# Performance work log

Hardware: AMD Instinct MI355X
Metric: run time of the kernel (lower is better)

The kernel has to match this reference:

```python
import jax, jax.numpy as jnp
import numpy as np

D_MODEL = 1024
N_HEADS = 16
D_K = D_MODEL // N_HEADS
D_FF = 4096
B, S = 4, 2048


def setup_inputs() -> dict:
    key = jax.random.key(0)
    ks = jax.random.split(key, 16)
    s = 0.02
    inp = {
        "x": jax.random.normal(ks[0], (B, S, D_MODEL), dtype=jnp.float32),
        "wq": jax.random.normal(ks[1], (D_MODEL, D_MODEL), dtype=jnp.float32) * s,
        "bq": jnp.zeros((D_MODEL,), jnp.float32),
        "wk": jax.random.normal(ks[2], (D_MODEL, D_MODEL), dtype=jnp.float32) * s,
        "bk": jnp.zeros((D_MODEL,), jnp.float32),
        "wv": jax.random.normal(ks[3], (D_MODEL, D_MODEL), dtype=jnp.float32) * s,
        "bv": jnp.zeros((D_MODEL,), jnp.float32),
        "wo": jax.random.normal(ks[4], (D_MODEL, D_MODEL), dtype=jnp.float32) * s,
        "bo": jnp.zeros((D_MODEL,), jnp.float32),
        "w1": jax.random.normal(ks[5], (D_MODEL, D_FF), dtype=jnp.float32) * s,
        "b1": jnp.zeros((D_FF,), jnp.float32),
        "w2": jax.random.normal(ks[6], (D_FF, D_MODEL), dtype=jnp.float32) * s,
        "b2": jnp.zeros((D_MODEL,), jnp.float32),
        "ln1_g": jnp.ones((D_MODEL,), jnp.float32),
        "ln1_b": jnp.zeros((D_MODEL,), jnp.float32),
        "ln2_g": jnp.ones((D_MODEL,), jnp.float32),
        "ln2_b": jnp.zeros((D_MODEL,), jnp.float32),
    }
    return inp


def _layernorm(x, g, b, eps=1e-5):
    mu = jnp.mean(x, axis=-1, keepdims=True)
    var = jnp.mean(jnp.square(x - mu), axis=-1, keepdims=True)
    return (x - mu) * jax.lax.rsqrt(var + eps) * g + b


def _attention(h, wq, bq, wk, bk, wv, bv, wo, bo):
    b, s, _ = h.shape
    q = (h @ wq + bq).reshape(b, s, N_HEADS, D_K).transpose(0, 2, 1, 3)
    k = (h @ wk + bk).reshape(b, s, N_HEADS, D_K).transpose(0, 2, 1, 3)
    v = (h @ wv + bv).reshape(b, s, N_HEADS, D_K).transpose(0, 2, 1, 3)
    scores = jnp.einsum('bhqd,bhkd->bhqk', q, k) / jnp.sqrt(jnp.float32(D_K))
    causal = jnp.triu(jnp.ones((s, s), dtype=bool), k=1)  # True above diag
    scores = jnp.where(causal[None, None], -jnp.inf, scores)
    attn = jax.nn.softmax(scores, axis=-1)
    out = jnp.einsum('bhqk,bhkd->bhqd', attn, v)
    out = out.transpose(0, 2, 1, 3).reshape(b, s, D_MODEL)
    return out @ wo + bo


def reference(x, wq, bq, wk, bk, wv, bv, wo, bo, w1, b1, w2, b2,
              ln1_g, ln1_b, ln2_g, ln2_b):
    attn_out = _attention(_layernorm(x, ln1_g, ln1_b), wq, bq, wk, bk, wv, bv, wo, bo)
    x = x + attn_out
    h = _layernorm(x, ln2_g, ln2_b)
    ff = jax.nn.gelu(h @ w1 + b1, approximate=False) @ w2 + b2
    return x + ff
```

## Files before the change

### kernel.cpp

```cpp
#include <hip/hip_runtime.h>
#include <hip/hip_bf16.h>

#define DM   1024
#define DFF  4096
#define NB   4
#define SS   2048
#define NH   16
#define DK   64
#define MROWS (NB*SS)

typedef __attribute__((ext_vector_type(8)))  short bfx8;
typedef __attribute__((ext_vector_type(4)))  float fx4;
typedef __attribute__((ext_vector_type(16))) float fx16;
typedef unsigned int u32;
typedef unsigned short u16;

static __device__ __forceinline__ u16 f2bf(float f) {
  union { __hip_bfloat16 h; u16 u; } cv;
  cv.h = __float2bfloat16(f);
  return cv.u;
}
static __device__ __forceinline__ u32 pk2bf(float a, float b) {
  return (u32)f2bf(a) | ((u32)f2bf(b) << 16);
}

static __device__ __forceinline__ void async16(void* lds, const void* g) {
  typedef const __attribute__((address_space(1))) unsigned int* gp_t;
  typedef __attribute__((address_space(3))) unsigned int* lp_t;
  __builtin_amdgcn_global_load_lds((gp_t)g, (lp_t)lds, 16, 0, 0);
}

__global__ __launch_bounds__(256) void k_transpose_all(
    const float* __restrict__ wq, const float* __restrict__ wk,
    const float* __restrict__ wv, const float* __restrict__ wo,
    const float* __restrict__ w1, const float* __restrict__ w2,
    u16* __restrict__ wqkv, u16* __restrict__ wot,
    u16* __restrict__ w1t,  u16* __restrict__ w2t) {
  __shared__ float t[32][33];
  const int idx = blockIdx.x;
  const float* in; u16* out; int K, N, bx, by;
  if (idx < 4096) {
    const int m = idx >> 10, tl = idx & 1023;
    in  = (m == 0) ? wq : (m == 1) ? wk : (m == 2) ? wv : wo;
    out = (m < 3) ? (wqkv + (size_t)m * 1024 * 1024) : wot;
    K = 1024; N = 1024; bx = tl & 31; by = tl >> 5;
  } else if (idx < 8192) {
    const int tl = idx - 4096;
    in = w1; out = w1t; K = 1024; N = 4096; bx = tl & 127; by = tl >> 7;
  } else {
    const int tl = idx - 8192;
    in = w2; out = w2t; K = 4096; N = 1024; bx = tl & 31; by = tl >> 5;
  }
  const int n0 = bx * 32, k0 = by * 32;
  const int tx = threadIdx.x & 31, ty = threadIdx.x >> 5;
#pragma unroll
  for (int j = 0; j < 4; j++)
    t[ty + j * 8][tx] = in[(size_t)(k0 + ty + j * 8) * N + n0 + tx];
  __syncthreads();
#pragma unroll
  for (int j = 0; j < 4; j++)
    out[(size_t)(n0 + ty + j * 8) * K + k0 + tx] = f2bf(t[tx][ty + j * 8]);
}

__global__ __launch_bounds__(256) void k_layernorm(const float* __restrict__ x,
                                                   const float* __restrict__ g,
                                                   const float* __restrict__ b,
                                                   u16* __restrict__ out) {
  const int row  = blockIdx.x * 4 + (threadIdx.x >> 6);
  const int lane = threadIdx.x & 63;
  const float* xr = x + (size_t)row * DM;
  float4 vb[4];
  float s = 0.f, s2 = 0.f;
#pragma unroll
  for (int j = 0; j < 4; j++) {
    float4 v = *(const float4*)(xr + j * 256 + lane * 4);
    vb[j] = v;
    s  += v.x + v.y + v.z + v.w;
    s2 += v.x * v.x + v.y * v.y + v.z * v.z + v.w * v.w;
  }
#pragma unroll
  for (int off = 1; off < 64; off <<= 1) {
    s  += __shfl_xor(s,  off);
    s2 += __shfl_xor(s2, off);
  }
  const float mu   = s * (1.f / DM);
  const float var  = s2 * (1.f / DM) - mu * mu;
  const float rstd = rsqrtf(var + 1e-5f);
  u16* orow = out + (size_t)row * DM;
#pragma unroll
  for (int j = 0; j < 4; j++) {
    const int col = j * 256 + lane * 4;
    uint2 o;
    o.x = pk2bf((vb[j].x - mu) * rstd * g[col + 0] + b[col + 0],
                (vb[j].y - mu) * rstd * g[col + 1] + b[col + 1]);
    o.y = pk2bf((vb[j].z - mu) * rstd * g[col + 2] + b[col + 2],
                (vb[j].w - mu) * rstd * g[col + 3] + b[col + 3]);
    *(uint2*)(orow + col) = o;
  }
}

template <int EPI>
__global__ __launch_bounds__(512, 2) void k_gemm256(const u16* __restrict__ A,
                                                    const u16* __restrict__ BT,
                                                    const float* __restrict__ bias0,
                                                    const float* __restrict__ bias1,
                                                    const float* __restrict__ bias2,
                                                    void* __restrict__ outp,
                                                    int M, int N, int K) {
  __shared__ char Sl[131072];

  const int tid = threadIdx.x, wave = tid >> 6, lane = tid & 63;
  const int nwg = gridDim.x * gridDim.y;
  const int bid = blockIdx.y * gridDim.x + blockIdx.x;
  const int swz = (bid & 7) * (nwg >> 3) + (bid >> 3);
  const int m0 = (swz / gridDim.x) * 256, n0 = (swz % gridDim.x) * 256;
  const int wr = wave >> 2, wcn = wave & 3;
  const int la = lane & 15, lg = lane >> 4;
  const int psw = (la >> 1) & 3;

  fx4 acc[8][4];
#pragma unroll
  for (int i = 0; i < 8; i++)
#pragma unroll
    for (int j = 0; j < 4; j++) acc[i][j] = fx4{0.f, 0.f, 0.f, 0.f};

  const int rp  = wave * 16 + (lane >> 2);
  const int sl  = (lane & 3) ^ ((lane >> 3) & 3);
  const int gra = (rp >> 6) * 128 + (rp & 63);
  const int grb = (rp >> 5) * 64 + (rp & 31);

  auto stageA = [&](int buf, int mh, int kt) {
    const u16* src = A + (size_t)(m0 + gra + mh * 64) * K + kt + sl * 8;
    char* dst = Sl + buf * 32768 + mh * 16384 + wave * 1024;
    async16(dst,        src);
    async16(dst + 8192, src + 32);
  };
  auto stageB = [&](int buf, int nh, int kt) {
    const u16* src = BT + (size_t)(n0 + grb + nh * 32) * K + kt + sl * 8;
    char* dst = Sl + 65536 + buf * 32768 + nh * 16384 + wave * 1024;
    async16(dst,        src);
    async16(dst + 8192, src + 32);
  };

  const int nk = K >> 6;
  stageA(0, 0, 0); stageB(0, 0, 0); stageA(0, 1, 0); stageB(0, 1, 0);
  asm volatile("s_waitcnt vmcnt(4)" ::: "memory");
  __builtin_amdgcn_sched_barrier(0);
  __builtin_amdgcn_s_barrier();
  asm volatile("" ::: "memory");

  bfx8 avv[4][2], bv0[2][2], bv1[2][2];

  auto readA = [&](int buf, int mh) {
    const char* base = Sl + buf * 32768 + mh * 16384;
#pragma unroll
    for (int mtl = 0; mtl < 4; mtl++) {
      const int r = wr * 64 + mtl * 16 + la;
#pragma unroll
      for (int kk = 0; kk < 2; kk++)
        avv[mtl][kk] = *(const bfx8*)(base + kk * 8192 + r * 64 + ((lg ^ psw) * 16));
    }
  };
  auto readB = [&](int buf, int nh, bfx8 (&bv)[2][2]) {
    const char* base = Sl + 65536 + buf * 32768 + nh * 16384;
#pragma unroll
    for (int ntl = 0; ntl < 2; ntl++) {
      const int r = wcn * 32 + ntl * 16 + la;
#pragma unroll
      for (int kk = 0; kk < 2; kk++)
        bv[ntl][kk] = *(const bfx8*)(base + kk * 8192 + r * 64 + ((lg ^ psw) * 16));
    }
  };
  auto quad = [&](int mh, int nh, bfx8 (&bv)[2][2]) {
    __builtin_amdgcn_s_setprio(1);
#pragma unroll
    for (int kk = 0; kk < 2; kk++)
#pragma unroll
      for (int mtl = 0; mtl < 4; mtl++)
#pragma unroll
        for (int ntl = 0; ntl < 2; ntl++)
          acc[mh * 4 + mtl][nh * 2 + ntl] = __builtin_amdgcn_mfma_f32_16x16x32_bf16(
              avv[mtl][kk], bv[ntl][kk], acc[mh * 4 + mtl][nh * 2 + ntl], 0, 0, 0);
    __builtin_amdgcn_s_setprio(0);
  };

#define PH_BAR_PRE()  do { __builtin_amdgcn_sched_barrier(0); __builtin_amdgcn_s_barrier(); \
                           asm volatile("s_waitcnt lgkmcnt(0)" ::: "memory");                \
                           __builtin_amdgcn_sched_barrier(0); } while (0)
#define PH_BAR_POST() do { __builtin_amdgcn_sched_barrier(0); __builtin_amdgcn_s_barrier(); \
                           asm volatile("" ::: "memory"); } while (0)

#pragma unroll 1
  for (int t = 0; t < nk; ++t) {
    const int buf = t & 1, nbuf = buf ^ 1;
    const bool pf = (t + 1 < nk);
    const int nkt = (t + 1) << 6;
    readA(buf, 0);
    readB(buf, 0, bv0);
    if (pf) stageA(nbuf, 0, nkt);
    PH_BAR_PRE();
    quad(0, 0, bv0);
    PH_BAR_POST();
    readB(buf, 1, bv1);
    if (pf) stageB(nbuf, 0, nkt);
    if (pf) { asm volatile("s_waitcnt vmcnt(4)" ::: "memory"); }
    else    { asm volatile("s_waitcnt vmcnt(0)" ::: "memory"); }
    PH_BAR_PRE();
    quad(0, 1, bv1);
    PH_BAR_POST();
    readA(buf, 1);
    if (pf) stageA(nbuf, 1, nkt);
    PH_BAR_PRE();
    quad(1, 0, bv0);
    PH_BAR_POST();
    if (pf) {
      stageB(nbuf, 1, nkt);
      asm volatile("s_waitcnt vmcnt(4)" ::: "memory");
    }
    PH_BAR_PRE();
    quad(1, 1, bv1);
    PH_BAR_POST();
  }
  __syncthreads();

  const int wm = wr * 128, wn = wcn * 64;
  float* scr = (float*)(void*)Sl + (size_t)wave * (68 * 16);

  auto emit_bf16 = [&](u16* base, size_t ld, int mrow0, int ncol0,
                       const float v[4][4] ) {
#pragma unroll
    for (int nt = 0; nt < 4; nt++)
#pragma unroll
      for (int vv = 0; vv < 4; vv++)
        scr[(lg * 4 + vv) * 68 + nt * 16 + la] = v[nt][vv];
    asm volatile("s_waitcnt lgkmcnt(0)" ::: "memory");
    __builtin_amdgcn_sched_barrier(0);
#pragma unroll
    for (int p = 0; p < 4; p++) {
      const int r  = p * 4 + (lane >> 4);
      const int cg = lane & 15;
      float4 q = *(const float4*)&scr[r * 68 + cg * 4];
      uint2 o;
      o.x = pk2bf(q.x, q.y);
      o.y = pk2bf(q.z, q.w);
      *(uint2*)(base + (size_t)(mrow0 + r) * ld + ncol0 + cg * 4) = o;
    }
    asm volatile("s_waitcnt lgkmcnt(0)" ::: "memory");
    __builtin_amdgcn_sched_barrier(0);
  };

  if constexpr (EPI == 4) {
    const int reg = n0 >> 10;
    const float* bp = (reg == 0) ? bias0 : (reg == 1) ? bias1 : bias2;
    if (reg < 2) {
      u16* base = (u16*)outp + (size_t)reg * (8u * 1024 * 1024);
#pragma unroll
      for (int mt = 0; mt < 8; mt++) {
        float v[4][4];
#pragma unroll
        for (int nt = 0; nt < 4; nt++) {
          const float bs = bp[(n0 + wn + nt * 16 + la) & 1023];
#pragma unroll
          for (int vv = 0; vv < 4; vv++) v[nt][vv] = acc[mt][nt][vv] + bs;
        }
        emit_bf16(base, 1024, m0 + wm + mt * 16, (n0 + wn) & 1023, v);
      }
    } else {
#pragma unroll
      for (int nt = 0; nt < 4; nt++) {
        const int nl = (n0 + wn + nt * 16 + la) & 1023;
        const float bs = bp[nl];
        const int hh = nl >> 6, d = nl & 63;
#pragma unroll
        for (int mt = 0; mt < 8; mt++) {
          const int m = m0 + wm + mt * 16 + lg * 4;
          const int bb2 = m >> 11, s = m & 2047;
          u16* vp = (u16*)outp + 16u * 1024 * 1024 +
                    (((size_t)bb2 * NH + hh) * DK + d) * SS + s;
          uint2 o;
          o.x = pk2bf(acc[mt][nt][0] + bs, acc[mt][nt][1] + bs);
          o.y = pk2bf(acc[mt][nt][2] + bs, acc[mt][nt][3] + bs);
          *(uint2*)vp = o;
        }
      }
    }
  } else {
#pragma unroll
    for (int mt = 0; mt < 8; mt++) {
      float v[4][4];
#pragma unroll
      for (int nt = 0; nt < 4; nt++) {
        const float bs = bias0[n0 + wn + nt * 16 + la];
#pragma unroll
        for (int vv = 0; vv < 4; vv++) {
          const float val = acc[mt][nt][vv] + bs;
          v[nt][vv] = 0.5f * val * (1.f + erff(val * 0.70710678118f));
        }
      }
      emit_bf16((u16*)outp, N, m0 + wm + mt * 16, n0 + wn, v);
    }
  }
#undef PH_BAR_PRE
#undef PH_BAR_POST
}

template <int EPI>
__global__ __launch_bounds__(512, 4) void k_gemm_bt(const u16* __restrict__ A,
                                                    const u16* __restrict__ BT,
                                                    const float* __restrict__ bias0,
                                                    const float* __restrict__ res,
                                                    void* __restrict__ outp,
                                                    int M, int N, int K) {
  constexpr int ABUF = 256 * 32 * 2;
  constexpr int BBUF = 128 * 32 * 2;
  __shared__ char Al[3 * ABUF];
  __shared__ char Bl[3 * BBUF];

  const int tid = threadIdx.x, wave = tid >> 6, lane = tid & 63;
  const int nwg = gridDim.x * gridDim.y;
  const int bid = blockIdx.y * gridDim.x + blockIdx.x;
  const int swz = (bid & 7) * (nwg >> 3) + (bid >> 3);
  const int m0 = (swz / gridDim.x) * 256, n0 = (swz % gridDim.x) * 128;
  const int wm = (wave >> 1) * 64, wn = (wave & 1) * 64;
  const int l31 = lane & 31, l5 = lane >> 5;
  const int psw = (l31 >> 1) & 3;

  fx16 acc[2][2];
#pragma unroll
  for (int i = 0; i < 2; i++)
#pragma unroll
    for (int j = 0; j < 2; j++)
#pragma unroll
      for (int e = 0; e < 16; e++) acc[i][j][e] = 0.f;

  const int arow = tid >> 2;
  const int aslot = ((tid & 3) ^ ((tid >> 3) & 3)) * 8;
  const u16* gA = A  + (size_t)(m0 + arow) * K + aslot;
  const u16* gB = BT + (size_t)(n0 + arow) * K + aslot;

  auto stageAB = [&](int buf, int kt) {
    async16(Al + buf * ABUF + wave * 1024,        gA + kt);
    async16(Al + buf * ABUF + 8192 + wave * 1024, gA + (size_t)128 * K + kt);
    async16(Bl + buf * BBUF + wave * 1024,        gB + kt);
  };

  const int nk = K >> 5;
  stageAB(0, 0);
  stageAB(1, 32);
  asm volatile("s_waitcnt vmcnt(3)" ::: "memory");
  __builtin_amdgcn_sched_barrier(0);
  __builtin_amdgcn_s_barrier();
  asm volatile("" ::: "memory");

  int cur = 0;
  for (int t = 0; t < nk; ++t) {
    const char* Ab = (const char*)Al + cur * ABUF;
    const char* Bb = (const char*)Bl + cur * BBUF;
    bfx8 av[2][2], bv[2][2];
#pragma unroll
    for (int mi = 0; mi < 2; mi++)
#pragma unroll
      for (int kk = 0; kk < 2; kk++)
        av[mi][kk] = *(const bfx8*)(Ab + (wm + mi * 32 + l31) * 64 +
                                    (((kk << 1) | l5) ^ psw) * 16);
#pragma unroll
    for (int ni = 0; ni < 2; ni++)
#pragma unroll
      for (int kk = 0; kk < 2; kk++)
        bv[ni][kk] = *(const bfx8*)(Bb + (wn + ni * 32 + l31) * 64 +
                                    (((kk << 1) | l5) ^ psw) * 16);
    int nb = cur + 2; if (nb >= 3) nb -= 3;
    if (t + 2 < nk) stageAB(nb, (t + 2) << 5);

    __builtin_amdgcn_s_setprio(1);
#pragma unroll
    for (int kk = 0; kk < 2; kk++)
#pragma unroll
      for (int mi = 0; mi < 2; mi++)
#pragma unroll
        for (int ni = 0; ni < 2; ni++)
          acc[mi][ni] = __builtin_amdgcn_mfma_f32_32x32x16_bf16(
              av[mi][kk], bv[ni][kk], acc[mi][ni], 0, 0, 0);
    __builtin_amdgcn_s_setprio(0);

    const int rem = nk - 1 - t;
    if (rem >= 2)      { asm volatile("s_waitcnt vmcnt(3)" ::: "memory"); }
    else if (rem == 1) { asm volatile("s_waitcnt vmcnt(0)" ::: "memory"); }
    __builtin_amdgcn_sched_barrier(0);
    if (rem > 0) __builtin_amdgcn_s_barrier();
    asm volatile("" ::: "memory");
    cur = (cur + 1 == 3) ? 0 : cur + 1;
  }

#pragma unroll
  for (int ni = 0; ni < 2; ni++) {
    const int n = n0 + wn + ni * 32 + l31;
    const float bs = bias0[n];
#pragma unroll
    for (int mi = 0; mi < 2; mi++) {
#pragma unroll
      for (int r = 0; r < 16; r++) {
        const int row = (r & 3) + 8 * (r >> 2) + 4 * l5;
        const size_t idx = (size_t)(m0 + wm + mi * 32 + row) * N + n;
        ((float*)outp)[idx] = res[idx] + acc[mi][ni][r] + bs;
      }
    }
  }
}

__global__ __launch_bounds__(512, 4) void k_attn(const u16* __restrict__ q,
                                                 const u16* __restrict__ k,
                                                 const u16* __restrict__ vt,
                                                 u16* __restrict__ att) {
  __shared__ char sm[65536];
  const int bid = blockIdx.x;
  const int bq = 15 - (bid >> 6);
  const int bh = bid & 63;
  const int b = bh >> 4, h = bh & 15;

  const int tid = threadIdx.x, wave = tid >> 6, lane = tid & 63;
  const int g = wave >> 2, wv4 = wave & 3;
  const int la = lane & 15, lg = lane >> 4;
  const int q0 = bq * 128;

  bfx8 qf[2][2];
#pragma unroll
  for (int qt = 0; qt < 2; qt++) {
    const u16* qp = q + (size_t)(b * SS + q0 + wv4 * 32 + qt * 16 + la) * DM + h * DK + lg * 8;
#pragma unroll
    for (int f = 0; f < 2; f++) qf[qt][f] = *(const bfx8*)(qp + f * 32);
  }

  fx4 acc[2][4];
#pragma unroll
  for (int qt = 0; qt < 2; qt++)
#pragma unroll
    for (int dt = 0; dt < 4; dt++) acc[qt][dt] = fx4{0.f, 0.f, 0.f, 0.f};
  float mold[2] = {-10000.f, -10000.f};
  float lsum[2] = {0.f, 0.f};

  const int srow = lane >> 3;
  const int sslot = (lane & 7) ^ srow;
  const u16* kg0 = k  + (size_t)(b * SS + wv4 * 16 + srow) * DM + h * DK + sslot * 8;
  const u16* vg0 = vt + (size_t)((b * NH + h) * DK + wv4 * 16 + srow) * SS + sslot * 8;
  char* kbase = sm + g * 32768 + wv4 * 2048;
  char* vbase = sm + g * 32768 + 16384 + wv4 * 2048;

  const float c1 = 0.18033688f;
  const int niter = bq + 1;

  auto stage = [&](int buf, int i) {
    const int c0 = (2 * i + g) * 64;
#pragma unroll
    for (int j = 0; j < 2; j++)
      async16(kbase + buf * 8192 + j * 1024, kg0 + (size_t)(c0 + j * 8) * DM);
#pragma unroll
    for (int j = 0; j < 2; j++)
      async16(vbase + buf * 8192 + j * 1024, vg0 + (size_t)(j * 8) * SS + c0);
  };

  stage(0, 0);
  int cur = 0;
  const int sw = la & 7;

  for (int i = 0; i < niter; i++) {
    __syncthreads();
    if (i + 1 < niter) stage(cur ^ 1, i + 1);
    const int c0 = (2 * i + g) * 64;
    const bool msk = (i == niter - 1);
    const char* Kb = sm + g * 32768 + cur * 8192;
    const char* Vb = sm + g * 32768 + 16384 + cur * 8192;

    fx4 st[2][4];
    __builtin_amdgcn_s_setprio(1);
#pragma unroll
    for (int t = 0; t < 4; t++) {
      const char* kr = Kb + (size_t)(t * 16 + la) * 128;
      bfx8 kf0 = *(const bfx8*)(kr + ((0 + lg) ^ sw) * 16);
      bfx8 kf1 = *(const bfx8*)(kr + ((4 + lg) ^ sw) * 16);
#pragma unroll
      for (int qt = 0; qt < 2; qt++) {
        fx4 z = fx4{0.f, 0.f, 0.f, 0.f};
        z = __builtin_amdgcn_mfma_f32_16x16x32_bf16(kf0, qf[qt][0], z, 0, 0, 0);
        z = __builtin_amdgcn_mfma_f32_16x16x32_bf16(kf1, qf[qt][1], z, 0, 0, 0);
        st[qt][t] = z;
      }
    }
    __builtin_amdgcn_s_setprio(0);

    if (msk) {
#pragma unroll
      for (int qt = 0; qt < 2; qt++) {
        const int qir = q0 + wv4 * 32 + qt * 16 + la;
#pragma unroll
        for (int t = 0; t < 4; t++)
#pragma unroll
          for (int r = 0; r < 4; r++)
            if (c0 + t * 16 + lg * 4 + r > qir) st[qt][t][r] = -1e9f;
      }
    }

    float lmx[2];
#pragma unroll
    for (int qt = 0; qt < 2; qt++) {
      float mx = fmaxf(fmaxf(st[qt][0][0], st[qt][0][1]), fmaxf(st[qt][0][2], st[qt][0][3]));
#pragma unroll
      for (int t = 1; t < 4; t++)
        mx = fmaxf(mx, fmaxf(fmaxf(st[qt][t][0], st[qt][t][1]), fmaxf(st[qt][t][2], st[qt][t][3])));
      lmx[qt] = mx * c1;
    }
    const bool def = (lmx[0] <= mold[0] + 8.f) && (lmx[1] <= mold[1] + 8.f);
    if (!__all(def)) {
#pragma unroll
      for (int qt = 0; qt < 2; qt++) {
        float mx = lmx[qt];
        mx = fmaxf(mx, __shfl_xor(mx, 16));
        mx = fmaxf(mx, __shfl_xor(mx, 32));
        const float mnew  = fmaxf(mold[qt], mx);
        const float scale = exp2f(mold[qt] - mnew);
        mold[qt] = mnew;
        lsum[qt] *= scale;
#pragma unroll
        for (int dt = 0; dt < 4; dt++) {
          acc[qt][dt][0] *= scale; acc[qt][dt][1] *= scale;
          acc[qt][dt][2] *= scale; acc[qt][dt][3] *= scale;
        }
      }
    }
    u32 W[2][4][2];
#pragma unroll
    for (int qt = 0; qt < 2; qt++) {
      float ps = 0.f;
#pragma unroll
      for (int t = 0; t < 4; t++) {
        float p0 = exp2f(fmaf(st[qt][t][0], c1, -mold[qt]));
        float p1 = exp2f(fmaf(st[qt][t][1], c1, -mold[qt]));
        float p2 = exp2f(fmaf(st[qt][t][2], c1, -mold[qt]));
        float p3 = exp2f(fmaf(st[qt][t][3], c1, -mold[qt]));
        ps += (p0 + p1) + (p2 + p3);
        W[qt][t][0] = pk2bf(p0, p1);
        W[qt][t][1] = pk2bf(p2, p3);
      }
      lsum[qt] += ps;
    }

    const int sLo = la + ((lg & 1) << 5);
    const int sHi = sLo + 16;
    const bool tHi = (lg >> 1) & 1;
#pragma unroll
    for (int f = 0; f < 2; f++) {
      bfx8 pf[2];
#pragma unroll
      for (int qt = 0; qt < 2; qt++) {
        const u32 a0 = __shfl(W[qt][2 * f][0], sLo), b0 = __shfl(W[qt][2 * f + 1][0], sLo);
        const u32 a1 = __shfl(W[qt][2 * f][1], sLo), b1 = __shfl(W[qt][2 * f + 1][1], sLo);
        const u32 a2 = __shfl(W[qt][2 * f][0], sHi), b2 = __shfl(W[qt][2 * f + 1][0], sHi);
        const u32 a3 = __shfl(W[qt][2 * f][1], sHi), b3 = __shfl(W[qt][2 * f + 1][1], sHi);
        union { u32 u[4]; bfx8 v; } pu;
        pu.u[0] = tHi ? b0 : a0;
        pu.u[1] = tHi ? b1 : a1;
        pu.u[2] = tHi ? b2 : a2;
        pu.u[3] = tHi ? b3 : a3;
        pf[qt] = pu.v;
      }
      __builtin_amdgcn_s_setprio(1);
#pragma unroll
      for (int dt = 0; dt < 4; dt++) {
        const int row = dt * 16 + la;
        bfx8 vf = *(const bfx8*)(Vb + (size_t)row * 128 + (((f << 2) + lg) ^ sw) * 16);
        acc[0][dt] = __builtin_amdgcn_mfma_f32_16x16x32_bf16(vf, pf[0], acc[0][dt], 0, 0, 0);
        acc[1][dt] = __builtin_amdgcn_mfma_f32_16x16x32_bf16(vf, pf[1], acc[1][dt], 0, 0, 0);
      }
      __builtin_amdgcn_s_setprio(0);
    }
    cur ^= 1;
  }

#pragma unroll
  for (int qt = 0; qt < 2; qt++) {
    lsum[qt] += __shfl_xor(lsum[qt], 16);
    lsum[qt] += __shfl_xor(lsum[qt], 32);
  }

  __syncthreads();
  const int gi = wv4 * 64 + lane;
  float* scr = (float*)sm + (size_t)gi * 36;
  if (g == 1) {
#pragma unroll
    for (int qt = 0; qt < 2; qt++)
#pragma unroll
      for (int dt = 0; dt < 4; dt++)
#pragma unroll
        for (int j = 0; j < 4; j++) scr[qt * 16 + dt * 4 + j] = acc[qt][dt][j];
    scr[32] = mold[0]; scr[33] = mold[1];
    scr[34] = lsum[0]; scr[35] = lsum[1];
  }
  __syncthreads();
  if (g == 0) {
#pragma unroll
    for (int qt = 0; qt < 2; qt++) {
      const float mB = scr[32 + qt], lB = scr[34 + qt];
      const float mN = fmaxf(mold[qt], mB);
      const float sA = exp2f(mold[qt] - mN);
      const float sB = exp2f(mB - mN);
      const float inv = 1.f / (lsum[qt] * sA + lB * sB);
      u16* ob = att + (size_t)(b * SS + q0 + wv4 * 32 + qt * 16 + la) * DM + h * DK + lg * 4;
#pragma unroll
      for (int dt = 0; dt < 4; dt++) {
        float o0 = (acc[qt][dt][0] * sA + scr[qt * 16 + dt * 4 + 0] * sB) * inv;
        float o1 = (acc[qt][dt][1] * sA + scr[qt * 16 + dt * 4 + 1] * sB) * inv;
        float o2 = (acc[qt][dt][2] * sA + scr[qt * 16 + dt * 4 + 2] * sB) * inv;
        float o3 = (acc[qt][dt][3] * sA + scr[qt * 16 + dt * 4 + 3] * sB) * inv;
        uint2 o;
        o.x = pk2bf(o0, o1);
        o.y = pk2bf(o2, o3);
        *(uint2*)(ob + dt * 16) = o;
      }
    }
  }
}

extern "C" void kernel_launch(void* const* d_in, const int* in_sizes, int n_in,
                              void* d_out, int out_size, void* d_ws, size_t ws_size,
                              hipStream_t stream) {
  const float* x    = (const float*)d_in[0];
  const float* wq   = (const float*)d_in[1];
  const float* bq   = (const float*)d_in[2];
  const float* wk   = (const float*)d_in[3];
  const float* bk   = (const float*)d_in[4];
  const float* wv   = (const float*)d_in[5];
  const float* bv   = (const float*)d_in[6];
  const float* wo   = (const float*)d_in[7];
  const float* bo   = (const float*)d_in[8];
  const float* w1   = (const float*)d_in[9];
  const float* b1   = (const float*)d_in[10];
  const float* w2   = (const float*)d_in[11];
  const float* b2   = (const float*)d_in[12];
  const float* ln1g = (const float*)d_in[13];
  const float* ln1b = (const float*)d_in[14];
  const float* ln2g = (const float*)d_in[15];
  const float* ln2b = (const float*)d_in[16];
  float* out = (float*)d_out;

  char* w = (char*)d_ws;
  const size_t MB = 1024ull * 1024ull;
  u16*   wqkv = (u16*)(w + 0 * MB);
  u16*   wot  = (u16*)(w + 6 * MB);
  u16*   w1t  = (u16*)(w + 8 * MB);
  u16*   w2t  = (u16*)(w + 16 * MB);
  float* x2   = (float*)(w + 24 * MB);
  u16*   hb   = (u16*)(w + 56 * MB);
  u16*   qb   = (u16*)(w + 72 * MB);
  u16*   kb   = (u16*)(w + 88 * MB);
  u16*   vtb  = (u16*)(w + 104 * MB);
  u16*   atb  = (u16*)(w + 120 * MB);
  u16*   ffb  = (u16*)(w + 72 * MB);

  k_transpose_all<<<dim3(12288), 256, 0, stream>>>(wq, wk, wv, wo, w1, w2,
                                                   wqkv, wot, w1t, w2t);

  k_layernorm<<<MROWS / 4, 256, 0, stream>>>(x, ln1g, ln1b, hb);

  k_gemm256<4><<<dim3(12, 32), 512, 0, stream>>>(hb, wqkv, bq, bk, bv, qb,
                                                 MROWS, 3 * DM, DM);

  k_attn<<<dim3(1024), 512, 0, stream>>>(qb, kb, vtb, atb);

  k_gemm_bt<1><<<dim3(8, 32), 512, 0, stream>>>(atb, wot, bo, x, x2,
                                                MROWS, DM, DM);

  k_layernorm<<<MROWS / 4, 256, 0, stream>>>(x2, ln2g, ln2b, hb);

  k_gemm256<2><<<dim3(16, 32), 512, 0, stream>>>(hb, w1t, b1, nullptr, nullptr, ffb,
                                                 MROWS, DFF, DM);

  k_gemm_bt<1><<<dim3(8, 32), 512, 0, stream>>>(ffb, w2t, b2, x2, out,
                                                MROWS, DM, DFF);
}
```

Baseline: 431.1 us.

## Unify GEMMs into templated 256x128 kernel with 4-stage pipeline and 16x16 MFMA

Replaces the old 32x32-MFMA k_gemm_bt with a templated kernel using 16x16x32 MFMA, a 4-deep async LDS pipeline, and a configurable wave grid. The QKV projection moves from the 256x256 k_gemm256 kernel to this 256x128 tile kernel with more workgroups. The GELU-fused FFN1 GEMM stays on the old 256x256 kernel, now specialised as k_gemm256_gelu. The aim is better latency hiding and more parallelism for the QKV and residual GEMMs, at the cost of lower per-tile data reuse and an occupancy of 2 instead of 4 for the residual GEMMs.

```diff
diff --git a/kernel.cpp b/kernel.cpp
--- a/kernel.cpp
+++ b/kernel.cpp
@@ -9,9 +9,8 @@
 #define DK   64
 #define MROWS (NB*SS)
 
-typedef __attribute__((ext_vector_type(8)))  short bfx8;
-typedef __attribute__((ext_vector_type(4)))  float fx4;
-typedef __attribute__((ext_vector_type(16))) float fx16;
+typedef __attribute__((ext_vector_type(8))) short bfx8;
+typedef __attribute__((ext_vector_type(4))) float fx4;
 typedef unsigned int u32;
 typedef unsigned short u16;
 
@@ -99,14 +98,182 @@
   }
 }
 
-template <int EPI>
-__global__ __launch_bounds__(512, 2) void k_gemm256(const u16* __restrict__ A,
+template <int EPI, int NWR>
+__global__ __launch_bounds__(512, 2) void k_gemm_bt(const u16* __restrict__ A,
                                                     const u16* __restrict__ BT,
                                                     const float* __restrict__ bias0,
                                                     const float* __restrict__ bias1,
                                                     const float* __restrict__ bias2,
+                                                    const float* __restrict__ res,
                                                     void* __restrict__ outp,
                                                     int M, int N, int K) {
+  constexpr int NWC   = 8 / NWR;
+  constexpr int BN    = NWC * 64;
+  constexpr int MFRAG = 256 / NWR / 16;
+  constexpr int ABUF  = 256 * 32 * 2;
+  constexpr int BBUF  = BN * 32 * 2;
+  constexpr int SA    = 2;
+  constexpr int SB    = BBUF / 8192;
+  constexpr int S     = SA + SB;
+
+  __shared__ char Al[4 * ABUF];
+  __shared__ char Bl[4 * BBUF];
+
+  const int tid = threadIdx.x, wave = tid >> 6, lane = tid & 63;
+  const int nwg = gridDim.x * gridDim.y;
+  const int bid = blockIdx.y * gridDim.x + blockIdx.x;
+  const int swz = (bid & 7) * (nwg >> 3) + (bid >> 3);
+  const int m0 = (swz / gridDim.x) * 256, n0 = (swz % gridDim.x) * BN;
+  const int wr = wave / NWC, wc = wave % NWC;
+  const int wm = wr * (256 / NWR), wn = wc * 64;
+  const int la = lane & 15, lg = lane >> 4;
+  const int psw = (la >> 1) & 3;
+
+  fx4 acc[MFRAG][4];
+#pragma unroll
+  for (int i = 0; i < MFRAG; i++)
+#pragma unroll
+    for (int j = 0; j < 4; j++) acc[i][j] = fx4{0.f, 0.f, 0.f, 0.f};
+
+  const int arow = tid >> 2;
+  const int aslot = ((tid & 3) ^ ((tid >> 3) & 3)) * 8;
+  const u16* gA = A  + (size_t)(m0 + arow) * K + aslot;
+  const u16* gB = BT + (size_t)(n0 + arow) * K + aslot;
+
+  auto stageA = [&](int buf, int kt) {
+#pragma unroll
+    for (int j = 0; j < SA; j++)
+      async16(Al + buf * ABUF + j * 8192 + wave * 1024, gA + (size_t)(j * 128) * K + kt);
+  };
+  auto stageB = [&](int buf, int kt) {
+#pragma unroll
+    for (int j = 0; j < SB; j++)
+      async16(Bl + buf * BBUF + j * 8192 + wave * 1024, gB + (size_t)(j * 128) * K + kt);
+  };
+
+  const int nk = K >> 5;
+  stageA(0, 0);  stageB(0, 0);
+  stageA(1, 32); stageB(1, 32);
+  stageA(2, 64); stageB(2, 64);
+  asm volatile("s_waitcnt vmcnt(%0)" :: "n"(2 * S) : "memory");
+  __builtin_amdgcn_s_barrier();
+  asm volatile("" ::: "memory");
+
+  for (int t = 0; t < nk; ++t) {
+    const char* Ab = (const char*)Al + (t & 3) * ABUF;
+    const char* Bb = (const char*)Bl + (t & 3) * BBUF;
+    const int rem = nk - 1 - t;
+    const bool pf = (t + 3 < nk);
+    const int pb = (t + 3) & 3;
+    const int pk = (t + 3) << 5;
+
+    bfx8 av[MFRAG], bv[4];
+#pragma unroll
+    for (int i = 0; i < MFRAG; i++)
+      av[i] = *(const bfx8*)(Ab + (wm + i * 16 + la) * 64 + (lg ^ psw) * 16);
+#pragma unroll
+    for (int i = 0; i < 4; i++)
+      bv[i] = *(const bfx8*)(Bb + (wn + i * 16 + la) * 64 + (lg ^ psw) * 16);
+    if (pf) { stageA(pb, pk); stageB(pb, pk); }
+    asm volatile("" ::: "memory");
+    __builtin_amdgcn_s_barrier();
+    asm volatile("" ::: "memory");
+    __builtin_amdgcn_s_setprio(1);
+#pragma unroll
+    for (int mt = 0; mt < MFRAG; mt++)
+#pragma unroll
+      for (int nt = 0; nt < 4; nt++)
+        acc[mt][nt] = __builtin_amdgcn_mfma_f32_16x16x32_bf16(av[mt], bv[nt], acc[mt][nt], 0, 0, 0);
+    __builtin_amdgcn_s_setprio(0);
+    if (rem >= 3)      { asm volatile("s_waitcnt vmcnt(%0)" :: "n"(2 * S) : "memory"); }
+    else if (rem == 2) { asm volatile("s_waitcnt vmcnt(%0)" :: "n"(S)     : "memory"); }
+    else if (rem == 1) { asm volatile("s_waitcnt vmcnt(0)" ::: "memory"); }
+    asm volatile("" ::: "memory");
+    __builtin_amdgcn_s_barrier();
+    asm volatile("" ::: "memory");
+  }
+
+  float* scr = (float*)(void*)Al + (size_t)wave * (68 * 16);
+
+  auto emit_bf16 = [&](u16* base, size_t ld, int mrow0, int ncol0,
+                       const float v[4][4]) {
+#pragma unroll
+    for (int nt = 0; nt < 4; nt++)
+#pragma unroll
+      for (int vv = 0; vv < 4; vv++)
+        scr[(lg * 4 + vv) * 68 + nt * 16 + la] = v[nt][vv];
+    asm volatile("s_waitcnt lgkmcnt(0)" ::: "memory");
+#pragma unroll
+    for (int p = 0; p < 4; p++) {
+      const int r  = p * 4 + (lane >> 4);
+      const int cg = lane & 15;
+      float4 q = *(const float4*)&scr[r * 68 + cg * 4];
+      uint2 o;
+      o.x = pk2bf(q.x, q.y);
+      o.y = pk2bf(q.z, q.w);
+      *(uint2*)(base + (size_t)(mrow0 + r) * ld + ncol0 + cg * 4) = o;
+    }
+    asm volatile("s_waitcnt lgkmcnt(0)" ::: "memory");
+  };
+
+  if constexpr (EPI == 4) {
+    const int reg = n0 >> 10;
+    const float* bp = (reg == 0) ? bias0 : (reg == 1) ? bias1 : bias2;
+    if (reg < 2) {
+      u16* base = (u16*)outp + (size_t)reg * (8u * 1024 * 1024);
+#pragma unroll
+      for (int mt = 0; mt < MFRAG; mt++) {
+        float v[4][4];
+#pragma unroll
+        for (int nt = 0; nt < 4; nt++) {
+          const float bs = bp[(n0 + wn + nt * 16 + la) & 1023];
+#pragma unroll
+          for (int vv = 0; vv < 4; vv++) v[nt][vv] = acc[mt][nt][vv] + bs;
+        }
+        emit_bf16(base, 1024, m0 + wm + mt * 16, (n0 + wn) & 1023, v);
+      }
+    } else {
+#pragma unroll
+      for (int nt = 0; nt < 4; nt++) {
+        const int nl = (n0 + wn + nt * 16 + la) & 1023;
+        const float bs = bp[nl];
+        const int hh = nl >> 6, d = nl & 63;
+#pragma unroll
+        for (int mt = 0; mt < MFRAG; mt++) {
+          const int m = m0 + wm + mt * 16 + lg * 4;
+          const int bb2 = m >> 11, s = m & 2047;
+          u16* vp = (u16*)outp + 16u * 1024 * 1024 +
+                    (((size_t)bb2 * NH + hh) * DK + d) * SS + s;
+          uint2 o;
+          o.x = pk2bf(acc[mt][nt][0] + bs, acc[mt][nt][1] + bs);
+          o.y = pk2bf(acc[mt][nt][2] + bs, acc[mt][nt][3] + bs);
+          *(uint2*)vp = o;
+        }
+      }
+    }
+  } else {
+#pragma unroll
+    for (int nt = 0; nt < 4; nt++) {
+      const int n = n0 + wn + nt * 16 + la;
+      const float bs = bias0[n];
+#pragma unroll
+      for (int mt = 0; mt < MFRAG; mt++) {
+#pragma unroll
+        for (int vv = 0; vv < 4; vv++) {
+          const int m = m0 + wm + mt * 16 + lg * 4 + vv;
+          const size_t idx = (size_t)m * N + n;
+          ((float*)outp)[idx] = res[idx] + acc[mt][nt][vv] + bs;
+        }
+      }
+    }
+  }
+}
+
+__global__ __launch_bounds__(512, 2) void k_gemm256_gelu(const u16* __restrict__ A,
+                                                         const u16* __restrict__ BT,
+                                                         const float* __restrict__ bias0,
+                                                         void* __restrict__ outp,
+                                                         int M, int N, int K) {
   __shared__ char Sl[131072];
 
   const int tid = threadIdx.x, wave = tid >> 6, lane = tid & 63;
@@ -226,8 +393,18 @@
   const int wm = wr * 128, wn = wcn * 64;
   float* scr = (float*)(void*)Sl + (size_t)wave * (68 * 16);
 
-  auto emit_bf16 = [&](u16* base, size_t ld, int mrow0, int ncol0,
-                       const float v[4][4] ) {
+#pragma unroll
+  for (int mt = 0; mt < 8; mt++) {
+    float v[4][4];
+#pragma unroll
+    for (int nt = 0; nt < 4; nt++) {
+      const float bs = bias0[n0 + wn + nt * 16 + la];
+#pragma unroll
+      for (int vv = 0; vv < 4; vv++) {
+        const float val = acc[mt][nt][vv] + bs;
+        v[nt][vv] = 0.5f * val * (1.f + erff(val * 0.70710678118f));
+      }
+    }
 #pragma unroll
     for (int nt = 0; nt < 4; nt++)
 #pragma unroll
@@ -243,169 +420,13 @@
       uint2 o;
       o.x = pk2bf(q.x, q.y);
       o.y = pk2bf(q.z, q.w);
-      *(uint2*)(base + (size_t)(mrow0 + r) * ld + ncol0 + cg * 4) = o;
+      *(uint2*)((u16*)outp + (size_t)(m0 + wm + mt * 16 + r) * N + n0 + wn + cg * 4) = o;
     }
     asm volatile("s_waitcnt lgkmcnt(0)" ::: "memory");
     __builtin_amdgcn_sched_barrier(0);
-  };
-
-  if constexpr (EPI == 4) {
-    const int reg = n0 >> 10;
-    const float* bp = (reg == 0) ? bias0 : (reg == 1) ? bias1 : bias2;
-    if (reg < 2) {
-      u16* base = (u16*)outp + (size_t)reg * (8u * 1024 * 1024);
-#pragma unroll
-      for (int mt = 0; mt < 8; mt++) {
-        float v[4][4];
-#pragma unroll
-        for (int nt = 0; nt < 4; nt++) {
-          const float bs = bp[(n0 + wn + nt * 16 + la) & 1023];
-#pragma unroll
-          for (int vv = 0; vv < 4; vv++) v[nt][vv] = acc[mt][nt][vv] + bs;
-        }
-        emit_bf16(base, 1024, m0 + wm + mt * 16, (n0 + wn) & 1023, v);
-      }
-    } else {
-#pragma unroll
-      for (int nt = 0; nt < 4; nt++) {
-        const int nl = (n0 + wn + nt * 16 + la) & 1023;
-        const float bs = bp[nl];
-        const int hh = nl >> 6, d = nl & 63;
-#pragma unroll
-        for (int mt = 0; mt < 8; mt++) {
-          const int m = m0 + wm + mt * 16 + lg * 4;
-          const int bb2 = m >> 11, s = m & 2047;
-          u16* vp = (u16*)outp + 16u * 1024 * 1024 +
-                    (((size_t)bb2 * NH + hh) * DK + d) * SS + s;
-          uint2 o;
-          o.x = pk2bf(acc[mt][nt][0] + bs, acc[mt][nt][1] + bs);
-          o.y = pk2bf(acc[mt][nt][2] + bs, acc[mt][nt][3] + bs);
-          *(uint2*)vp = o;
-        }
-      }
-    }
-  } else {
-#pragma unroll
-    for (int mt = 0; mt < 8; mt++) {
-      float v[4][4];
-#pragma unroll
-      for (int nt = 0; nt < 4; nt++) {
-        const float bs = bias0[n0 + wn + nt * 16 + la];
-#pragma unroll
-        for (int vv = 0; vv < 4; vv++) {
-          const float val = acc[mt][nt][vv] + bs;
-          v[nt][vv] = 0.5f * val * (1.f + erff(val * 0.70710678118f));
-        }
-      }
-      emit_bf16((u16*)outp, N, m0 + wm + mt * 16, n0 + wn, v);
-    }
   }
 #undef PH_BAR_PRE
 #undef PH_BAR_POST
-}
-
-template <int EPI>
-__global__ __launch_bounds__(512, 4) void k_gemm_bt(const u16* __restrict__ A,
-                                                    const u16* __restrict__ BT,
-                                                    const float* __restrict__ bias0,
-                                                    const float* __restrict__ res,
-                                                    void* __restrict__ outp,
-                                                    int M, int N, int K) {
-  constexpr int ABUF = 256 * 32 * 2;
-  constexpr int BBUF = 128 * 32 * 2;
-  __shared__ char Al[3 * ABUF];
-  __shared__ char Bl[3 * BBUF];
-
-  const int tid = threadIdx.x, wave = tid >> 6, lane = tid & 63;
-  const int nwg = gridDim.x * gridDim.y;
-  const int bid = blockIdx.y * gridDim.x + blockIdx.x;
-  const int swz = (bid & 7) * (nwg >> 3) + (bid >> 3);
-  const int m0 = (swz / gridDim.x) * 256, n0 = (swz % gridDim.x) * 128;
-  const int wm = (wave >> 1) * 64, wn = (wave & 1) * 64;
-  const int l31 = lane & 31, l5 = lane >> 5;
-  const int psw = (l31 >> 1) & 3;
-
-  fx16 acc[2][2];
-#pragma unroll
-  for (int i = 0; i < 2; i++)
-#pragma unroll
-    for (int j = 0; j < 2; j++)
-#pragma unroll
-      for (int e = 0; e < 16; e++) acc[i][j][e] = 0.f;
-
-  const int arow = tid >> 2;
-  const int aslot = ((tid & 3) ^ ((tid >> 3) & 3)) * 8;
-  const u16* gA = A  + (size_t)(m0 + arow) * K + aslot;
-  const u16* gB = BT + (size_t)(n0 + arow) * K + aslot;
-
-  auto stageAB = [&](int buf, int kt) {
-    async16(Al + buf * ABUF + wave * 1024,        gA + kt);
-    async16(Al + buf * ABUF + 8192 + wave * 1024, gA + (size_t)128 * K + kt);
-    async16(Bl + buf * BBUF + wave * 1024,        gB + kt);
-  };
-
-  const int nk = K >> 5;
-  stageAB(0, 0);
-  stageAB(1, 32);
-  asm volatile("s_waitcnt vmcnt(3)" ::: "memory");
-  __builtin_amdgcn_sched_barrier(0);
-  __builtin_amdgcn_s_barrier();
-  asm volatile("" ::: "memory");
-
-  int cur = 0;
-  for (int t = 0; t < nk; ++t) {
-    const char* Ab = (const char*)Al + cur * ABUF;
-    const char* Bb = (const char*)Bl + cur * BBUF;
-    bfx8 av[2][2], bv[2][2];
-#pragma unroll
-    for (int mi = 0; mi < 2; mi++)
-#pragma unroll
-      for (int kk = 0; kk < 2; kk++)
-        av[mi][kk] = *(const bfx8*)(Ab + (wm + mi * 32 + l31) * 64 +
-                                    (((kk << 1) | l5) ^ psw) * 16);
-#pragma unroll
-    for (int ni = 0; ni < 2; ni++)
-#pragma unroll
-      for (int kk = 0; kk < 2; kk++)
-        bv[ni][kk] = *(const bfx8*)(Bb + (wn + ni * 32 + l31) * 64 +
-                                    (((kk << 1) | l5) ^ psw) * 16);
-    int nb = cur + 2; if (nb >= 3) nb -= 3;
-    if (t + 2 < nk) stageAB(nb, (t + 2) << 5);
-
-    __builtin_amdgcn_s_setprio(1);
-#pragma unroll
-    for (int kk = 0; kk < 2; kk++)
-#pragma unroll
-      for (int mi = 0; mi < 2; mi++)
-#pragma unroll
-        for (int ni = 0; ni < 2; ni++)
-          acc[mi][ni] = __builtin_amdgcn_mfma_f32_32x32x16_bf16(
-              av[mi][kk], bv[ni][kk], acc[mi][ni], 0, 0, 0);
-    __builtin_amdgcn_s_setprio(0);
-
-    const int rem = nk - 1 - t;
-    if (rem >= 2)      { asm volatile("s_waitcnt vmcnt(3)" ::: "memory"); }
-    else if (rem == 1) { asm volatile("s_waitcnt vmcnt(0)" ::: "memory"); }
-    __builtin_amdgcn_sched_barrier(0);
-    if (rem > 0) __builtin_amdgcn_s_barrier();
-    asm volatile("" ::: "memory");
-    cur = (cur + 1 == 3) ? 0 : cur + 1;
-  }
-
-#pragma unroll
-  for (int ni = 0; ni < 2; ni++) {
-    const int n = n0 + wn + ni * 32 + l31;
-    const float bs = bias0[n];
-#pragma unroll
-    for (int mi = 0; mi < 2; mi++) {
-#pragma unroll
-      for (int r = 0; r < 16; r++) {
-        const int row = (r & 3) + 8 * (r >> 2) + 4 * l5;
-        const size_t idx = (size_t)(m0 + wm + mi * 32 + row) * N + n;
-        ((float*)outp)[idx] = res[idx] + acc[mi][ni][r] + bs;
-      }
-    }
-  }
 }
 
 __global__ __launch_bounds__(512, 4) void k_attn(const u16* __restrict__ q,
@@ -661,19 +682,19 @@
 
   k_layernorm<<<MROWS / 4, 256, 0, stream>>>(x, ln1g, ln1b, hb);
 
-  k_gemm256<4><<<dim3(12, 32), 512, 0, stream>>>(hb, wqkv, bq, bk, bv, qb,
-                                                 MROWS, 3 * DM, DM);
+  k_gemm_bt<4, 4><<<dim3(24, 32), 512, 0, stream>>>(hb, wqkv, bq, bk, bv, nullptr, qb,
+                                                    MROWS, 3 * DM, DM);
 
   k_attn<<<dim3(1024), 512, 0, stream>>>(qb, kb, vtb, atb);
 
-  k_gemm_bt<1><<<dim3(8, 32), 512, 0, stream>>>(atb, wot, bo, x, x2,
-                                                MROWS, DM, DM);
+  k_gemm_bt<1, 4><<<dim3(8, 32), 512, 0, stream>>>(atb, wot, bo, nullptr, nullptr, x, x2,
+                                                   MROWS, DM, DM);
 
   k_layernorm<<<MROWS / 4, 256, 0, stream>>>(x2, ln2g, ln2b, hb);
 
-  k_gemm256<2><<<dim3(16, 32), 512, 0, stream>>>(hb, w1t, b1, nullptr, nullptr, ffb,
-                                                 MROWS, DFF, DM);
-
-  k_gemm_bt<1><<<dim3(8, 32), 512, 0, stream>>>(ffb, w2t, b2, x2, out,
-                                                MROWS, DM, DFF);
-}
+  k_gemm256_gelu<<<dim3(16, 32), 512, 0, stream>>>(hb, w1t, b1, ffb,
+                                                   MROWS, DFF, DM);
+
+  k_gemm_bt<1, 4><<<dim3(8, 32), 512, 0, stream>>>(ffb, w2t, b2, nullptr, nullptr, x2, out,
+                                                   MROWS, DM, DFF);
+}
```

New measurement: 388.1 us. 1.11x faster.
